# Kernel optimization log

Measured on AMD Instinct MI355X. Metric: run time of the kernel, lower is better.

## Reference

```python
import jax, jax.numpy as jnp
import numpy as np
from jax import lax

B, U, D = 16, 2048, 512


def setup_inputs() -> dict:
    key = jax.random.key(0)
    ks = jax.random.split(key, 6)
    xs = jax.random.normal(ks[0], (B, U, D), dtype=jnp.float32)
    xlens = jax.random.randint(ks[1], (B,), U // 2, U + 1).astype(jnp.int32)
    ylens = jax.random.randint(ks[2], (B,), 128, 257).astype(jnp.int32)
    # Conv1d(D, D, kernel_size=3, padding=1): weight [O, I, K], bias [O]
    conv_w = jax.random.normal(ks[3], (D, D, 3), dtype=jnp.float32) * (1.0 / np.sqrt(3 * D))
    conv_b = jnp.zeros((D,), dtype=jnp.float32)
    # Linear(D, 1)
    lin_w = jax.random.normal(ks[4], (1, D), dtype=jnp.float32) * (1.0 / np.sqrt(D))
    lin_b = jnp.zeros((1,), dtype=jnp.float32)
    return {"xs": xs, "xlens": xlens, "ylens": ylens,
            "conv_w": conv_w, "conv_b": conv_b, "lin_w": lin_w, "lin_b": lin_b}


def _forward(xs, xlens, ylens, conv_w, conv_b, lin_w, lin_b, u_max):
    # alpha gate: conv1d -> relu -> linear -> sigmoid
    h = lax.conv_general_dilated(xs.transpose(0, 2, 1), conv_w, (1,), ((1, 1),),
                                 dimension_numbers=("NCH", "OIH", "NCH"))
    h = jax.nn.relu(h + conv_b[None, :, None])          # [B, D, U]
    alpha = jax.nn.sigmoid(jnp.einsum("bdu,od->bu", h, lin_w) + lin_b[0])  # [B, U]
    # zero padded positions (positions >= xlen)
    pos = jnp.arange(U)[None, :]
    alpha = jnp.where(pos >= xlens[:, None], 0.0, alpha)
    sum_alpha = alpha.sum(-1)                            # [B]
    beta = sum_alpha / ylens.astype(sum_alpha.dtype) - 1e-4  # [B]

    def step(carry, inp):
        prev_alpha, prev_state = carry                   # [B], [B, D]
        cur_alpha, cur_state = inp                       # [B], [B, D]
        new_alpha = prev_alpha + cur_alpha
        fired = new_alpha >= beta                        # [B]
        left = (beta - prev_alpha)[:, None]
        right = (new_alpha - beta)[:, None]
        integ = prev_state + left * cur_state            # integrated state at fire
        next_alpha = jnp.where(fired, right[:, 0], new_alpha)
        next_state = jnp.where(fired[:, None], right * cur_state, integ)
        next_fired = jnp.where(fired[:, None], integ, jnp.zeros_like(integ))
        return (next_alpha, next_state), next_fired

    init = (jnp.zeros((B,), xs.dtype), jnp.zeros((B, D), xs.dtype))
    _, fired_seq = lax.scan(step, init, (alpha.T, xs.transpose(1, 0, 2)))
    fired_state = fired_seq.transpose(1, 0, 2)           # [B, U, D]

    # stable-move fired frames to the front of each batch row
    marks = jnp.abs(fired_state).sum(-1) != 0.0          # [B, U] bool
    order = jnp.argsort(~marks, axis=1, stable=True)     # fired (False-key) first
    cif_output = jnp.take_along_axis(fired_state, order[:, :, None], axis=1)
    h_cif = cif_output[:, :u_max, :]
    return h_cif, sum_alpha


def reference(xs, xlens, ylens, conv_w, conv_b, lin_w, lin_b):
    u_max = int(jnp.max(ylens))
    return _forward(xs, xlens, ylens, conv_w, conv_b, lin_w, lin_b, u_max)
```

## Files before the change

kernel.cpp:

```cpp
#include <hip/hip_runtime.h>
#include <cstddef>
#include <cstdint>

#define Bb 16
#define Uu 2048
#define Dd 512
#define BU (Bb*Uu)

typedef short bf16x8 __attribute__((ext_vector_type(8)));
typedef float f32x4 __attribute__((ext_vector_type(4)));

#define ROW_BYTES 144
#define A_BYTES 18720
#define B_SLICE 18432
#define B_BASE (2*A_BYTES)
#define STEP_BYTES (512*ROW_BYTES)
#define SMEM_BYTES (B_BASE + 2*B_SLICE)

#define WAITVM(N) asm volatile("s_waitcnt vmcnt(" #N ")" ::: "memory")
#define WAITLGKM0 asm volatile("s_waitcnt lgkmcnt(0)" ::: "memory")

__device__ __forceinline__ unsigned short f2bf(float x){
  unsigned int u = __float_as_uint(x);
  u += 0x7fff + ((u >> 16) & 1);
  return (unsigned short)(u >> 16);
}
__device__ __forceinline__ float bf2f(unsigned short b){
  return __uint_as_float(((unsigned int)b) << 16);
}

union U16x8 { unsigned short s[8]; uint4 v; };

__device__ __forceinline__ void split2(float x, unsigned short& h, unsigned short& m){
  h = f2bf(x);
  float r1 = x - bf2f(h);
  m = f2bf(r1);
}

__global__ __launch_bounds__(256) void pack_b_kernel(const float* __restrict__ conv_w,
                                                     char* __restrict__ Bpack){
  int idx = blockIdx.x * 256 + threadIdx.x;
  int n = idx >> 6, cg = idx & 63;
  int chunk = cg >> 2, sub = cg & 3, c0 = cg << 3;
  const float* src = conv_w + (size_t)n * (Dd * 3) + (size_t)c0 * 3;
  float w[24];
  #pragma unroll
  for (int j = 0; j < 24; ++j) w[j] = src[j];
  #pragma unroll
  for (int tap = 0; tap < 3; ++tap){
    U16x8 H, M;
    #pragma unroll
    for (int j = 0; j < 8; ++j) split2(w[j * 3 + tap], H.s[j], M.s[j]);
    char* dst = Bpack + (size_t)(chunk * 3 + tap) * STEP_BYTES + n * ROW_BYTES + sub * 16;
    *(uint4*)dst = H.v;
    *(uint4*)(dst + 64) = M.v;
  }
}

__device__ __forceinline__ void stage_A_direct(char* abuf, const float* __restrict__ xsb,
                                               int u0, int c0, int tid){
  #pragma unroll
  for (int it = 0; it < 3; ++it){
    if (it < 2 || tid < 8){
      int t = (it < 2) ? (tid + it * 256) : (512 + tid);
      int r = t >> 2, cg = t & 3;
      int uu = u0 - 1 + r;
      float x[8];
      if (uu >= 0 && uu < Uu){
        const float* p = xsb + (size_t)uu * Dd + c0 + cg * 8;
        float4 a = *(const float4*)p;
        float4 b = *(const float4*)(p + 4);
        x[0]=a.x; x[1]=a.y; x[2]=a.z; x[3]=a.w; x[4]=b.x; x[5]=b.y; x[6]=b.z; x[7]=b.w;
      } else {
        #pragma unroll
        for (int j = 0; j < 8; ++j) x[j] = 0.f;
      }
      U16x8 H, M;
      #pragma unroll
      for (int j = 0; j < 8; ++j) split2(x[j], H.s[j], M.s[j]);
      char* dst = abuf + r * ROW_BYTES + cg * 16;
      *(uint4*)(dst)      = H.v;
      *(uint4*)(dst + 64) = M.v;
    }
  }
}

__device__ __forceinline__ void gll16(const char* g, char* l){
  __builtin_amdgcn_global_load_lds(
      (const __attribute__((address_space(1))) unsigned int*)g,
      (__attribute__((address_space(3))) unsigned int*)l, 16, 0, 0);
}

__device__ __forceinline__ void stage_slice(char* ldsB, const char* __restrict__ src,
                                            int lane, int wv){
  const char* g = src + wv * 1024 + lane * 16;
  char* l = ldsB + wv * 1024;
  gll16(g, l);
  gll16(g + 4096,  l + 4096);
  gll16(g + 8192,  l + 8192);
  gll16(g + 12288, l + 12288);
  if (wv < 2) gll16(g + 16384, l + 16384);
}

__device__ __forceinline__ bf16x8 ldfrag(const char* p){
  return __builtin_bit_cast(bf16x8, *(const uint4*)p);
}

__global__ __launch_bounds__(256, 2) void conv_mfma_full_kernel(
    const float* __restrict__ xs, const char* __restrict__ Bpack,
    const float* __restrict__ conv_b, const float* __restrict__ lin_w,
    const int* __restrict__ xlens,
    float* __restrict__ partial)
{
  __shared__ __align__(16) char smem[SMEM_BYTES];
  const int tid = threadIdx.x;
  const int lane = tid & 63, wv = tid >> 6;
  const int wm = wv >> 1;
  const int wn = wv & 1;
  const int ut = blockIdx.x >> 6;
  const int cs = (blockIdx.x >> 4) & 3;
  const int b  = blockIdx.x & 15;
  const int u0 = ut * 128;
  if (u0 >= xlens[b]) return;
  const float* xsb = xs + (size_t)b * Uu * Dd;
  const int li = lane & 15, lg = lane >> 4;

  f32x4 acc[4][4];
  #pragma unroll
  for (int m = 0; m < 4; ++m)
    #pragma unroll
    for (int n = 0; n < 4; ++n){
      f32x4 z = {0.f, 0.f, 0.f, 0.f};
      acc[m][n] = z;
    }

  stage_A_direct(smem, xsb, u0, 0, tid);
  stage_slice(smem + B_BASE, Bpack + cs * B_SLICE, lane, wv);
  __syncthreads();

  for (int chunk = 0; chunk < 16; ++chunk){
    const bool more = (chunk < 15);
    const char* aC = smem + (chunk & 1) * A_BYTES;
    char* aN = smem + ((chunk & 1) ^ 1) * A_BYTES;

    bf16x8 a[4][2];
    #pragma unroll
    for (int m = 0; m < 4; ++m){
      const char* ar = aC + (size_t)(wm * 64 + m * 16 + li) * ROW_BYTES + lg * 16;
      a[m][0] = ldfrag(ar);
      a[m][1] = ldfrag(ar + 64);
    }

    #pragma unroll
    for (int tap = 0; tap < 3; ++tap){
      const int p = chunk * 3 + tap;
      const int bbuf = p & 1;
      const bool apf_now = (tap == 2) && more;

      float4 pa0, pa1, pb0, pb1, pe0, pe1;
      int rA = 0, cgA = 0;
      if (apf_now){
        const float4 z4 = make_float4(0.f,0.f,0.f,0.f);
        pa0 = z4; pa1 = z4; pe0 = z4; pe1 = z4;
        int c0n = (chunk + 1) * 32;
        rA = tid >> 2; cgA = tid & 3;
        int uuA = u0 - 1 + rA;
        if (uuA >= 0){
          const float* pp = xsb + (size_t)uuA * Dd + c0n + cgA * 8;
          pa0 = *(const float4*)pp;
          pa1 = *(const float4*)(pp + 4);
        }
        {
          const float* pp = xsb + (size_t)(u0 + 63 + rA) * Dd + c0n + cgA * 8;
          pb0 = *(const float4*)pp;
          pb1 = *(const float4*)(pp + 4);
        }
        if (wv == 0){
          int rE = 128 + (lane >> 2);
          int uuE = u0 - 1 + rE;
          if (lane < 8 && uuE < Uu){
            const float* pp = xsb + (size_t)uuE * Dd + c0n + (lane & 3) * 8;
            pe0 = *(const float4*)pp;
            pe1 = *(const float4*)(pp + 4);
          }
        }
        __builtin_amdgcn_sched_barrier(0);
      }

      if (p < 47)
        stage_slice(smem + B_BASE + (bbuf ^ 1) * B_SLICE,
                    Bpack + (size_t)(p + 1) * STEP_BYTES + cs * B_SLICE, lane, wv);

      if (p == 47)            { WAITVM(0); }
      else if (apf_now)       { if (wv == 0) WAITVM(11); else if (wv == 1) WAITVM(9); else WAITVM(8); }
      else                    { if (wv < 2) WAITVM(5); else WAITVM(4); }
      __builtin_amdgcn_sched_barrier(0);

      __builtin_amdgcn_s_setprio(1);
      const char* bbase = smem + B_BASE + bbuf * B_SLICE;
      #pragma unroll
      for (int n = 0; n < 4; ++n){
        const char* br = bbase + (size_t)(wn * 64 + n * 16 + li) * ROW_BYTES + lg * 16;
        bf16x8 bh = ldfrag(br);
        bf16x8 bm = ldfrag(br + 64);
        #pragma unroll
        for (int m = 0; m < 4; ++m) acc[m][n] = __builtin_amdgcn_mfma_f32_16x16x32_bf16(a[m][0], bh, acc[m][n], 0, 0, 0);
        #pragma unroll
        for (int m = 0; m < 4; ++m) acc[m][n] = __builtin_amdgcn_mfma_f32_16x16x32_bf16(a[m][1], bh, acc[m][n], 0, 0, 0);
        #pragma unroll
        for (int m = 0; m < 4; ++m) acc[m][n] = __builtin_amdgcn_mfma_f32_16x16x32_bf16(a[m][0], bm, acc[m][n], 0, 0, 0);
        #pragma unroll
        for (int m = 0; m < 4; ++m) acc[m][n] = __builtin_amdgcn_mfma_f32_16x16x32_bf16(a[m][1], bm, acc[m][n], 0, 0, 0);
      }
      __builtin_amdgcn_s_setprio(0);

      if (tap < 2){
        #pragma unroll
        for (int m = 0; m < 4; ++m){
          const char* ar = aC + (size_t)(wm * 64 + m * 16 + li + tap + 1) * ROW_BYTES + lg * 16;
          a[m][0] = ldfrag(ar);
          a[m][1] = ldfrag(ar + 64);
        }
      }

      if (apf_now){
        if (wv < 2) { WAITVM(5); } else { WAITVM(4); }
        __builtin_amdgcn_sched_barrier(0);
        U16x8 H, M;
        float x[8];
        x[0]=pa0.x; x[1]=pa0.y; x[2]=pa0.z; x[3]=pa0.w;
        x[4]=pa1.x; x[5]=pa1.y; x[6]=pa1.z; x[7]=pa1.w;
        #pragma unroll
        for (int jj = 0; jj < 8; ++jj) split2(x[jj], H.s[jj], M.s[jj]);
        char* dst = aN + rA * ROW_BYTES + cgA * 16;
        *(uint4*)(dst)      = H.v;
        *(uint4*)(dst + 64) = M.v;
        x[0]=pb0.x; x[1]=pb0.y; x[2]=pb0.z; x[3]=pb0.w;
        x[4]=pb1.x; x[5]=pb1.y; x[6]=pb1.z; x[7]=pb1.w;
        #pragma unroll
        for (int jj = 0; jj < 8; ++jj) split2(x[jj], H.s[jj], M.s[jj]);
        char* dst2 = aN + (64 + rA) * ROW_BYTES + cgA * 16;
        *(uint4*)(dst2)      = H.v;
        *(uint4*)(dst2 + 64) = M.v;
        if (wv == 0){
          if (lane < 8){
            float y[8];
            y[0]=pe0.x; y[1]=pe0.y; y[2]=pe0.z; y[3]=pe0.w;
            y[4]=pe1.x; y[5]=pe1.y; y[6]=pe1.z; y[7]=pe1.w;
            #pragma unroll
            for (int jj = 0; jj < 8; ++jj) split2(y[jj], H.s[jj], M.s[jj]);
            char* dst3 = aN + (128 + (lane >> 2)) * ROW_BYTES + (lane & 3) * 16;
            *(uint4*)(dst3)      = H.v;
            *(uint4*)(dst3 + 64) = M.v;
          }
        }
        WAITLGKM0;
        __builtin_amdgcn_sched_barrier(0);
      }
      __builtin_amdgcn_s_barrier();
    }
  }

  __syncthreads();
  float* pbuf = (float*)smem;
  #pragma unroll
  for (int m = 0; m < 4; ++m){
    float s0 = 0.f, s1 = 0.f, s2 = 0.f, s3 = 0.f;
    #pragma unroll
    for (int n = 0; n < 4; ++n){
      int col = cs * 128 + wn * 64 + n * 16 + li;
      float cb = conv_b[col], lw = lin_w[col];
      f32x4 v = acc[m][n];
      float h;
      h = v[0] + cb; h = h > 0.f ? h : 0.f; s0 += h * lw;
      h = v[1] + cb; h = h > 0.f ? h : 0.f; s1 += h * lw;
      h = v[2] + cb; h = h > 0.f ? h : 0.f; s2 += h * lw;
      h = v[3] + cb; h = h > 0.f ? h : 0.f; s3 += h * lw;
    }
    #pragma unroll
    for (int msk = 1; msk < 16; msk <<= 1){
      s0 += __shfl_xor(s0, msk); s1 += __shfl_xor(s1, msk);
      s2 += __shfl_xor(s2, msk); s3 += __shfl_xor(s3, msk);
    }
    if (li == 0){
      int fr = wm * 64 + m * 16 + lg * 4;
      pbuf[(fr + 0) * 2 + wn] = s0;
      pbuf[(fr + 1) * 2 + wn] = s1;
      pbuf[(fr + 2) * 2 + wn] = s2;
      pbuf[(fr + 3) * 2 + wn] = s3;
    }
  }
  __syncthreads();
  if (tid < 128){
    float pv = pbuf[tid * 2] + pbuf[tid * 2 + 1];
    partial[(size_t)cs * BU + (size_t)b * Uu + u0 + tid] = pv;
  }
}

__global__ __launch_bounds__(64) void scan_kernel(
    const float* __restrict__ partial, const float* __restrict__ lin_b,
    const int* __restrict__ xlens, const int* __restrict__ ylens,
    float* __restrict__ wA, float* __restrict__ wB,
    int* __restrict__ fire_pos, int* __restrict__ nf,
    float* __restrict__ out_sum)
{
  __shared__ float salpha[Uu];
  int b = blockIdx.x;
  int lane = threadIdx.x;
  int xl = xlens[b];
  int xce = (xl + 63) & ~63;
  float lb = lin_b[0];

  float sum = 0.f;
  for (int u0 = 0; u0 < xce; u0 += 64){
    int u = u0 + lane;
    size_t ix = (size_t)b * Uu + u;
    float v = lb + partial[ix] + partial[BU + ix] + partial[2 * BU + ix] + partial[3 * BU + ix];
    float a = 1.f / (1.f + expf(-v));
    if (u >= xl) a = 0.f;
    salpha[u] = a;
    sum += a;
  }
  #pragma unroll
  for (int m = 1; m < 64; m <<= 1) sum += __shfl_xor(sum, m);
  float sa = sum;
  float beta = sa / (float)ylens[b] - 1e-4f;
  if (lane == 0) out_sum[b] = sa;

  float prev = 0.f;
  int cnt = 0;
  for (int u0 = 0; u0 < Uu; u0 += 64) {
    if (u0 >= xl) break;
    float val = salpha[u0 + lane];
    float mywa = 0.f, mywb = 0.f;
    #pragma unroll
    for (int i = 0; i < 64; ++i) {
      float a_cur = __builtin_bit_cast(float,
          __builtin_amdgcn_readlane(__builtin_bit_cast(int, val), i));
      float nw = prev + a_cur;
      float left = beta - prev;
      float right = nw - beta;
      bool fired = nw >= beta;
      if (lane == i) { mywa = left; mywb = right; }
      if (fired) {
        if (lane == 0) fire_pos[(b << 11) + cnt] = u0 + i;
        ++cnt;
      }
      prev = fired ? right : nw;
    }
    wA[(size_t)b * Uu + u0 + lane] = mywa;
    wB[(size_t)b * Uu + u0 + lane] = mywb;
  }
  if (lane == 0) nf[b] = cnt;
}

__global__ __launch_bounds__(512) void gather_kernel(
    const float* __restrict__ xs, const float* __restrict__ wA, const float* __restrict__ wB,
    const int* __restrict__ fire_pos, const int* __restrict__ nf,
    float* __restrict__ out, int umax)
{
  int t = blockIdx.x, b = blockIdx.y;
  int tid = threadIdx.x;
  float* o = out + ((size_t)b * umax + t) * Dd;
  int n = nf[b];
  if (t >= n) { o[tid] = 0.f; return; }
  int start = (t == 0) ? 0 : fire_pos[(b << 11) + t - 1];
  int end = fire_pos[(b << 11) + t];
  const float* xb = xs + (size_t)b * Uu * Dd;
  float acc = 0.f;
  for (int u = start; u <= end; ++u) {
    float w = (t > 0 && u == start) ? wB[(size_t)b * Uu + u] : wA[(size_t)b * Uu + u];
    acc += w * xb[(size_t)u * Dd + tid];
  }
  o[tid] = acc;
}

extern "C" void kernel_launch(void* const* d_in, const int* in_sizes, int n_in,
                              void* d_out, int out_size, void* d_ws, size_t ws_size,
                              hipStream_t stream) {
  const float* xs     = (const float*)d_in[0];
  const int*   xlens  = (const int*)d_in[1];
  const int*   ylens  = (const int*)d_in[2];
  const float* conv_w = (const float*)d_in[3];
  const float* conv_b = (const float*)d_in[4];
  const float* lin_w  = (const float*)d_in[5];
  const float* lin_b  = (const float*)d_in[6];
  float* out = (float*)d_out;
  int umax = (out_size - Bb) / (Bb * Dd);

  char* ws = (char*)d_ws;
  char*  Bpack    = ws;
  float* partial  = (float*)(ws + 48 * (size_t)STEP_BYTES);
  float* wAv      = partial + 4 * BU;
  float* wBv      = wAv + BU;
  int*   fire_pos = (int*)(wBv + BU);
  int*   nf       = (int*)(fire_pos + BU);

  pack_b_kernel<<<(512 * 64) / 256, 256, 0, stream>>>(conv_w, Bpack);
  conv_mfma_full_kernel<<<1024, 256, 0, stream>>>(xs, Bpack, conv_b, lin_w, xlens, partial);
  scan_kernel<<<Bb, 64, 0, stream>>>(partial, lin_b, xlens, ylens, wAv, wBv, fire_pos, nf,
                                     out + (size_t)Bb * umax * Dd);
  if (umax > 0)
    gather_kernel<<<dim3(umax, Bb), 512, 0, stream>>>(xs, wAv, wBv, fire_pos, nf, out, umax);
}
```

Measured before the change: 277.5 us.

## Repack A and B LDS tiles into fragment-contiguous planes without row padding

Changes the shared-memory layout of the bf16 hi/lo split operands. Rows move from 144-byte padded rows to per-lane-group planes where each MFMA fragment read is contiguous 16-byte accesses. This cuts LDS and packed-weight footprint, drops the extra fifth global-to-LDS load per slice, and spreads the edge-row prefetch evenly across waves so the vmcnt waits become uniform. The plane strides must still avoid LDS bank conflicts, otherwise fragment loads could serialize.

```diff
diff --git a/kernel.cpp b/kernel.cpp
--- a/kernel.cpp
+++ b/kernel.cpp
@@ -10,11 +10,12 @@
 typedef short bf16x8 __attribute__((ext_vector_type(8)));
 typedef float f32x4 __attribute__((ext_vector_type(4)));
 
-#define ROW_BYTES 144
-#define A_BYTES 18720
-#define B_SLICE 18432
-#define B_BASE (2*A_BYTES)
-#define STEP_BYTES (512*ROW_BYTES)
+#define A_PLANE 2080
+#define A_SPLIT 8320
+#define A_BYTES 16640
+#define B_SLICE 16384
+#define B_BASE  33280
+#define STEP_BYTES 65536
 #define SMEM_BYTES (B_BASE + 2*B_SLICE)
 
 #define WAITVM(N) asm volatile("s_waitcnt vmcnt(" #N ")" ::: "memory")
@@ -41,19 +42,21 @@
                                                      char* __restrict__ Bpack){
   int idx = blockIdx.x * 256 + threadIdx.x;
   int n = idx >> 6, cg = idx & 63;
-  int chunk = cg >> 2, sub = cg & 3, c0 = cg << 3;
+  int chunk = cg >> 2, lg = cg & 3, c0 = cg << 3;
   const float* src = conv_w + (size_t)n * (Dd * 3) + (size_t)c0 * 3;
   float w[24];
   #pragma unroll
   for (int j = 0; j < 24; ++j) w[j] = src[j];
+  int cs = n >> 7, cc = n & 127, cgrp = cc >> 4, li = cc & 15;
+  char* base = Bpack + (size_t)cs * B_SLICE + cgrp * 2048 + lg * 256 + li * 16;
   #pragma unroll
   for (int tap = 0; tap < 3; ++tap){
     U16x8 H, M;
     #pragma unroll
     for (int j = 0; j < 8; ++j) split2(w[j * 3 + tap], H.s[j], M.s[j]);
-    char* dst = Bpack + (size_t)(chunk * 3 + tap) * STEP_BYTES + n * ROW_BYTES + sub * 16;
+    char* dst = base + (size_t)(chunk * 3 + tap) * STEP_BYTES;
     *(uint4*)dst = H.v;
-    *(uint4*)(dst + 64) = M.v;
+    *(uint4*)(dst + 1024) = M.v;
   }
 }
 
@@ -63,11 +66,11 @@
   for (int it = 0; it < 3; ++it){
     if (it < 2 || tid < 8){
       int t = (it < 2) ? (tid + it * 256) : (512 + tid);
-      int r = t >> 2, cg = t & 3;
+      int r = t >> 2, lgw = t & 3;
       int uu = u0 - 1 + r;
       float x[8];
       if (uu >= 0 && uu < Uu){
-        const float* p = xsb + (size_t)uu * Dd + c0 + cg * 8;
+        const float* p = xsb + (size_t)uu * Dd + c0 + lgw * 8;
         float4 a = *(const float4*)p;
         float4 b = *(const float4*)(p + 4);
         x[0]=a.x; x[1]=a.y; x[2]=a.z; x[3]=a.w; x[4]=b.x; x[5]=b.y; x[6]=b.z; x[7]=b.w;
@@ -78,9 +81,9 @@
       U16x8 H, M;
       #pragma unroll
       for (int j = 0; j < 8; ++j) split2(x[j], H.s[j], M.s[j]);
-      char* dst = abuf + r * ROW_BYTES + cg * 16;
-      *(uint4*)(dst)      = H.v;
-      *(uint4*)(dst + 64) = M.v;
+      char* dst = abuf + lgw * A_PLANE + r * 16;
+      *(uint4*)(dst)           = H.v;
+      *(uint4*)(dst + A_SPLIT) = M.v;
     }
   }
 }
@@ -99,7 +102,6 @@
   gll16(g + 4096,  l + 4096);
   gll16(g + 8192,  l + 8192);
   gll16(g + 12288, l + 12288);
-  if (wv < 2) gll16(g + 16384, l + 16384);
 }
 
 __device__ __forceinline__ bf16x8 ldfrag(const char* p){
@@ -135,7 +137,7 @@
     }
 
   stage_A_direct(smem, xsb, u0, 0, tid);
-  stage_slice(smem + B_BASE, Bpack + cs * B_SLICE, lane, wv);
+  stage_slice(smem + B_BASE, Bpack + (size_t)cs * B_SLICE, lane, wv);
   __syncthreads();
 
   for (int chunk = 0; chunk < 16; ++chunk){
@@ -146,9 +148,9 @@
     bf16x8 a[4][2];
     #pragma unroll
     for (int m = 0; m < 4; ++m){
-      const char* ar = aC + (size_t)(wm * 64 + m * 16 + li) * ROW_BYTES + lg * 16;
+      const char* ar = aC + lg * A_PLANE + (size_t)(wm * 64 + m * 16 + li) * 16;
       a[m][0] = ldfrag(ar);
-      a[m][1] = ldfrag(ar + 64);
+      a[m][1] = ldfrag(ar + A_SPLIT);
     }
 
     #pragma unroll
@@ -158,51 +160,53 @@
       const bool apf_now = (tap == 2) && more;
 
       float4 pa0, pa1, pb0, pb1, pe0, pe1;
-      int rA = 0, cgA = 0;
+      int rA = 0, cgA = 0, rE = 0, lgE = 0;
+      bool aval = true, eval_ = true;
       if (apf_now){
         const float4 z4 = make_float4(0.f,0.f,0.f,0.f);
-        pa0 = z4; pa1 = z4; pe0 = z4; pe1 = z4;
         int c0n = (chunk + 1) * 32;
         rA = tid >> 2; cgA = tid & 3;
         int uuA = u0 - 1 + rA;
-        if (uuA >= 0){
-          const float* pp = xsb + (size_t)uuA * Dd + c0n + cgA * 8;
-          pa0 = *(const float4*)pp;
-          pa1 = *(const float4*)(pp + 4);
+        aval = (uuA >= 0);
+        int uuAc = aval ? uuA : 0;
+        const float* pp = xsb + (size_t)uuAc * Dd + c0n + cgA * 8;
+        pa0 = *(const float4*)pp;
+        pa1 = *(const float4*)(pp + 4);
+        if (!aval){ pa0 = z4; pa1 = z4; }
+        const float* pq = xsb + (size_t)(u0 + 63 + rA) * Dd + c0n + cgA * 8;
+        pb0 = *(const float4*)pq;
+        pb1 = *(const float4*)(pq + 4);
+        int q = wv * 2 + lane;
+        rE = 128 + (q >> 2); lgE = q & 3;
+        int uuE = u0 - 1 + rE;
+        eval_ = (uuE < Uu);
+        int uuEc = eval_ ? uuE : (Uu - 1);
+        pe0 = z4; pe1 = z4;
+        if (lane < 2){
+          const float* pr = xsb + (size_t)uuEc * Dd + c0n + lgE * 8;
+          pe0 = *(const float4*)pr;
+          pe1 = *(const float4*)(pr + 4);
         }
-        {
-          const float* pp = xsb + (size_t)(u0 + 63 + rA) * Dd + c0n + cgA * 8;
-          pb0 = *(const float4*)pp;
-          pb1 = *(const float4*)(pp + 4);
-        }
-        if (wv == 0){
-          int rE = 128 + (lane >> 2);
-          int uuE = u0 - 1 + rE;
-          if (lane < 8 && uuE < Uu){
-            const float* pp = xsb + (size_t)uuE * Dd + c0n + (lane & 3) * 8;
-            pe0 = *(const float4*)pp;
-            pe1 = *(const float4*)(pp + 4);
-          }
-        }
+        if (!eval_){ pe0 = z4; pe1 = z4; }
         __builtin_amdgcn_sched_barrier(0);
       }
 
       if (p < 47)
         stage_slice(smem + B_BASE + (bbuf ^ 1) * B_SLICE,
-                    Bpack + (size_t)(p + 1) * STEP_BYTES + cs * B_SLICE, lane, wv);
-
-      if (p == 47)            { WAITVM(0); }
-      else if (apf_now)       { if (wv == 0) WAITVM(11); else if (wv == 1) WAITVM(9); else WAITVM(8); }
-      else                    { if (wv < 2) WAITVM(5); else WAITVM(4); }
+                    Bpack + (size_t)(p + 1) * STEP_BYTES + (size_t)cs * B_SLICE, lane, wv);
+
+      if (p == 47)       { WAITVM(0); }
+      else if (apf_now)  { WAITVM(10); }
+      else               { WAITVM(4); }
       __builtin_amdgcn_sched_barrier(0);
 
       __builtin_amdgcn_s_setprio(1);
       const char* bbase = smem + B_BASE + bbuf * B_SLICE;
       #pragma unroll
       for (int n = 0; n < 4; ++n){
-        const char* br = bbase + (size_t)(wn * 64 + n * 16 + li) * ROW_BYTES + lg * 16;
+        const char* br = bbase + (size_t)(wn * 4 + n) * 2048 + lg * 256 + li * 16;
         bf16x8 bh = ldfrag(br);
-        bf16x8 bm = ldfrag(br + 64);
+        bf16x8 bm = ldfrag(br + 1024);
         #pragma unroll
         for (int m = 0; m < 4; ++m) acc[m][n] = __builtin_amdgcn_mfma_f32_16x16x32_bf16(a[m][0], bh, acc[m][n], 0, 0, 0);
         #pragma unroll
@@ -217,14 +221,14 @@
       if (tap < 2){
         #pragma unroll
         for (int m = 0; m < 4; ++m){
-          const char* ar = aC + (size_t)(wm * 64 + m * 16 + li + tap + 1) * ROW_BYTES + lg * 16;
+          const char* ar = aC + lg * A_PLANE + (size_t)(wm * 64 + m * 16 + li + tap + 1) * 16;
           a[m][0] = ldfrag(ar);
-          a[m][1] = ldfrag(ar + 64);
+          a[m][1] = ldfrag(ar + A_SPLIT);
         }
       }
 
       if (apf_now){
-        if (wv < 2) { WAITVM(5); } else { WAITVM(4); }
+        WAITVM(4);
         __builtin_amdgcn_sched_barrier(0);
         U16x8 H, M;
         float x[8];
@@ -232,27 +236,25 @@
         x[4]=pa1.x; x[5]=pa1.y; x[6]=pa1.z; x[7]=pa1.w;
         #pragma unroll
         for (int jj = 0; jj < 8; ++jj) split2(x[jj], H.s[jj], M.s[jj]);
-        char* dst = aN + rA * ROW_BYTES + cgA * 16;
-        *(uint4*)(dst)      = H.v;
-        *(uint4*)(dst + 64) = M.v;
+        char* dA = aN + cgA * A_PLANE + rA * 16;
+        *(uint4*)(dA)           = H.v;
+        *(uint4*)(dA + A_SPLIT) = M.v;
         x[0]=pb0.x; x[1]=pb0.y; x[2]=pb0.z; x[3]=pb0.w;
         x[4]=pb1.x; x[5]=pb1.y; x[6]=pb1.z; x[7]=pb1.w;
         #pragma unroll
         for (int jj = 0; jj < 8; ++jj) split2(x[jj], H.s[jj], M.s[jj]);
-        char* dst2 = aN + (64 + rA) * ROW_BYTES + cgA * 16;
-        *(uint4*)(dst2)      = H.v;
-        *(uint4*)(dst2 + 64) = M.v;
-        if (wv == 0){
-          if (lane < 8){
-            float y[8];
-            y[0]=pe0.x; y[1]=pe0.y; y[2]=pe0.z; y[3]=pe0.w;
-            y[4]=pe1.x; y[5]=pe1.y; y[6]=pe1.z; y[7]=pe1.w;
-            #pragma unroll
-            for (int jj = 0; jj < 8; ++jj) split2(y[jj], H.s[jj], M.s[jj]);
-            char* dst3 = aN + (128 + (lane >> 2)) * ROW_BYTES + (lane & 3) * 16;
-            *(uint4*)(dst3)      = H.v;
-            *(uint4*)(dst3 + 64) = M.v;
-          }
+        char* dB = aN + cgA * A_PLANE + (64 + rA) * 16;
+        *(uint4*)(dB)           = H.v;
+        *(uint4*)(dB + A_SPLIT) = M.v;
+        if (lane < 2){
+          float y[8];
+          y[0]=pe0.x; y[1]=pe0.y; y[2]=pe0.z; y[3]=pe0.w;
+          y[4]=pe1.x; y[5]=pe1.y; y[6]=pe1.z; y[7]=pe1.w;
+          #pragma unroll
+          for (int jj = 0; jj < 8; ++jj) split2(y[jj], H.s[jj], M.s[jj]);
+          char* dE = aN + lgE * A_PLANE + rE * 16;
+          *(uint4*)(dE)           = H.v;
+          *(uint4*)(dE + A_SPLIT) = M.v;
         }
         WAITLGKM0;
         __builtin_amdgcn_sched_barrier(0);
```

After: 280.3 us. No clear change (+1.0%).
